# Kernel optimization log

Measured on AMD Instinct MI355X. Metric: run time of the kernel, lower is better.

The kernel has to match this reference:

```python
import jax, jax.numpy as jnp
import numpy as np

# SpargeAttn / spas_sage2_attn_meansim block sizes
BLKQ, BLKK = 128, 64
NUM_HEADS = 8
SIMTHRESHD1 = 0.6
CDFTHRESHD = 0.98


def _block_meta(t, blk):
    # t: [B,H,S,D] -> block means [B,H,nb,D] and min-cosine-to-mean per block [B,H,nb]
    B, H, S, D = t.shape
    nb = S // blk
    tb = t.reshape(B, H, nb, blk, D)
    m = tb.mean(axis=3)
    tn = tb / (jnp.linalg.norm(tb, axis=-1, keepdims=True) + 1e-6)
    mn = m / (jnp.linalg.norm(m, axis=-1, keepdims=True) + 1e-6)
    cos = jnp.einsum('bhnkd,bhnd->bhnk', tn, mn)
    return m, cos.min(axis=-1)


def _meansim_sparse_attention(q, k, v, scale):
    # Block-sparse attention with mean-similarity pruning (SpargeAttn meansim).
    qm, qsim = _block_meta(q, BLKQ)          # [B,H,nq,D], [B,H,nq]
    km, ksim = _block_meta(k, BLKK)          # [B,H,nk,D], [B,H,nk]
    q_self = qsim > SIMTHRESHD1              # self-similar Q blocks -> mean is representative
    k_self = ksim > SIMTHRESHD1
    # pooled attention map over block means
    pooled = jax.nn.softmax(jnp.einsum('bhqd,bhkd->bhqk', qm, km) * scale, axis=-1)
    # per Q-block row: keep highest-prob K blocks until cumulative mass >= cdfthreshd
    order = jnp.argsort(-pooled, axis=-1)
    sp = jnp.take_along_axis(pooled, order, axis=-1)
    csum = jnp.cumsum(sp, axis=-1)
    keep_sorted = (csum - sp) < CDFTHRESHD   # always keeps at least the top block
    inv = jnp.argsort(order, axis=-1)
    keep = jnp.take_along_axis(keep_sorted, inv, axis=-1)  # [B,H,nq,nk]
    # conservative fallback: non-self-similar Q/K blocks are never pruned
    block_mask = keep | (~q_self)[..., None] | (~k_self)[:, :, None, :]
    tok_mask = jnp.repeat(jnp.repeat(block_mask, BLKQ, axis=2), BLKK, axis=3)
    s = jnp.einsum('bhqd,bhkd->bhqk', q, k) * scale
    s = jnp.where(tok_mask, s, -jnp.inf)
    p = jax.nn.softmax(s, axis=-1)
    return jnp.einsum('bhqk,bhkd->bhqd', p, v)


def setup_inputs() -> dict:
    key = jax.random.key(0)
    B, L, C = 2, 2048, 512
    ks = jax.random.split(key, 3)
    x = jax.random.normal(ks[0], (B, L, C), jnp.float32)
    Wqkv = jax.random.normal(ks[1], (C, 3 * C), jnp.float32) * (C ** -0.5)
    bqkv = jnp.zeros((3 * C,), jnp.float32)
    Wproj = jax.random.normal(ks[2], (C, C), jnp.float32) * (C ** -0.5)
    bproj = jnp.zeros((C,), jnp.float32)
    return {"x": x, "Wqkv": Wqkv, "bqkv": bqkv, "Wproj": Wproj, "bproj": bproj}


def reference(x, Wqkv, bqkv, Wproj, bproj):
    B, L, C = x.shape
    H = NUM_HEADS
    D = C // H
    scale = D ** -0.5
    qkv = (x @ Wqkv + bqkv).reshape(B, L, 3, H, D)
    qkv = jnp.transpose(qkv, (2, 0, 3, 1, 4))  # [3,B,H,L,D]
    q, k, v = qkv[0], qkv[1], qkv[2]
    o = _meansim_sparse_attention(q, k, v, scale)  # [B,H,L,D]
    o = jnp.transpose(o, (0, 2, 1, 3)).reshape(B, L, C)
    return o @ Wproj + bproj
```

## Files before the change

### kernel.cpp

```cpp
#include <hip/hip_runtime.h>
#include <math.h>

typedef unsigned short ushortT;
typedef unsigned int uintT;
typedef __attribute__((ext_vector_type(8))) short short8;
typedef __attribute__((ext_vector_type(16))) float f32x16;
#define MFMA32(a, b, c) __builtin_amdgcn_mfma_f32_32x32x16_bf16((a), (b), (c), 0, 0, 0)


#define LOG2E 1.4426950408889634f

static __device__ __forceinline__ ushortT f2b(float f) {
    union { float f; uintT u; } v; v.f = f;
    uintT u = v.u;
    u += 0x7fffu + ((u >> 16) & 1u);
    return (ushortT)(u >> 16);
}
static __device__ __forceinline__ uintT pack2(float a, float b) {
    return (uintT)f2b(a) | ((uintT)f2b(b) << 16);
}
static __device__ __forceinline__ uintT pack2t(float a, float b) {
    union { float f; uintT u; } x0, x1; x0.f = a; x1.f = b;
    return __builtin_amdgcn_perm(x1.u, x0.u, 0x07060302u);
}
static __device__ __forceinline__ float blo(uintT u) {
    union { uintT u; float f; } v; v.u = u << 16; return v.f;
}
static __device__ __forceinline__ float bhi(uintT u) {
    union { uintT u; float f; } v; v.u = u & 0xffff0000u; return v.f;
}
static __device__ __forceinline__ f32x16 zero16() {
    f32x16 z;
    #pragma unroll
    for (int i = 0; i < 16; ++i) z[i] = 0.f;
    return z;
}

#define NQB 16
#define NKB 32

__global__ __launch_bounds__(256) void prep_kernel(
    const float* __restrict__ x, ushortT* __restrict__ xb,
    const float* __restrict__ Wq, ushortT* __restrict__ Wqt,
    const float* __restrict__ Wp, ushortT* __restrict__ Wpt) {
    const int bid = blockIdx.x, t = threadIdx.x;
    __shared__ float tile[32][33];
    if (bid < 2048) {
        int i = (bid * 256 + t) * 4;
        float4 v = *(const float4*)(x + i);
        uint2 o; o.x = pack2(v.x, v.y); o.y = pack2(v.z, v.w);
        *(uint2*)(xb + i) = o;
        return;
    }
    const float* W; ushortT* Wt; int C, c0, r0;
    if (bid < 2816) {
        const int b = bid - 2048;
        W = Wq; Wt = Wqt; C = 1536;
        c0 = (b % 48) * 32; r0 = (b / 48) * 32;
    } else {
        const int b = bid - 2816;
        W = Wp; Wt = Wpt; C = 512;
        c0 = (b & 15) * 32; r0 = (b >> 4) * 32;
    }
    const int tx = t & 31, ty = t >> 5;
    #pragma unroll
    for (int i = 0; i < 4; ++i)
        tile[ty + 8 * i][tx] = W[(size_t)(r0 + ty + 8 * i) * C + c0 + tx];
    __syncthreads();
    #pragma unroll
    for (int i = 0; i < 4; ++i) {
        int rr = ty + 8 * i;
        Wt[(size_t)(c0 + rr) * 512 + r0 + tx] = f2b(tile[tx][rr]);
    }
}

__global__ __launch_bounds__(256) void qkv_gemm_kernel(
    const ushortT* __restrict__ xb, const ushortT* __restrict__ wt,
    const float* __restrict__ bias,
    ushortT* __restrict__ qb, ushortT* __restrict__ kfrag, ushortT* __restrict__ vfrag,
    float* __restrict__ qm, float* __restrict__ km,
    float* __restrict__ qs, float* __restrict__ ks) {
    __shared__ __align__(16) ushortT As[2][128 * 40];
    __shared__ __align__(16) ushortT Bs[2][64 * 40];
    __shared__ float sumbuf[4][64];
    __shared__ float meanS[2][64];
    __shared__ float wminS[4];
    const int t = threadIdx.x;
    const int l = t & 63, w = t >> 6;
    const int lm = l & 31, lh = l >> 5;
    const int rowbase = blockIdx.y * 128;
    const int colbase = blockIdx.x * 64;

    f32x16 acc[2];
    acc[0] = zero16(); acc[1] = zero16();

    const int r = t >> 1, half = t & 1;
    const ushortT* Ag = xb + (size_t)(rowbase + r) * 512 + half * 16;
    const int soA = r * 40 + half * 16;
    const int rb = t >> 2, q4 = t & 3;
    const ushortT* Bg = wt + (size_t)(colbase + rb) * 512 + q4 * 8;
    const int soB = rb * 40 + q4 * 8;

    uint4 a0, a1, b0;
    a0 = *(const uint4*)(Ag); a1 = *(const uint4*)(Ag + 8);
    b0 = *(const uint4*)(Bg);
    *(uint4*)(&As[0][soA]) = a0; *(uint4*)(&As[0][soA] + 8) = a1;
    *(uint4*)(&Bs[0][soB]) = b0;

    for (int k0 = 0; k0 < 512; k0 += 32) {
        const int cur = (k0 >> 5) & 1;
        __syncthreads();
        if (k0 < 480) {
            a0 = *(const uint4*)(Ag + k0 + 32); a1 = *(const uint4*)(Ag + k0 + 40);
            b0 = *(const uint4*)(Bg + k0 + 32);
        }
        #pragma unroll
        for (int ks2 = 0; ks2 < 2; ++ks2) {
            const int ko = 16 * ks2 + 8 * lh;
            short8 af  = *(const short8*)(&As[cur][(32 * w + lm) * 40 + ko]);
            short8 b_0 = *(const short8*)(&Bs[cur][lm * 40 + ko]);
            short8 b_1 = *(const short8*)(&Bs[cur][(32 + lm) * 40 + ko]);
            acc[0] = MFMA32(af, b_0, acc[0]);
            acc[1] = MFMA32(af, b_1, acc[1]);
        }
        if (k0 < 480) {
            const int nxt = cur ^ 1;
            *(uint4*)(&As[nxt][soA]) = a0; *(uint4*)(&As[nxt][soA] + 8) = a1;
            *(uint4*)(&Bs[nxt][soB]) = b0;
        }
    }

    const int which = blockIdx.x >> 3;
    const int h = blockIdx.x & 7;
    const int by = blockIdx.y;
    const int b = by >> 4;
    const size_t hb = (size_t)(b * 8 + h);
    float bias2[2];
    #pragma unroll
    for (int nt = 0; nt < 2; ++nt) bias2[nt] = bias[colbase + 32 * nt + lm];
    float msum[2] = {0.f, 0.f};
    #pragma unroll
    for (int nt = 0; nt < 2; ++nt) {
        const int dd = 32 * nt + lm;
        #pragma unroll
        for (int rg = 0; rg < 16; ++rg) {
            const int row_local = 32 * w + (rg & 3) + 8 * (rg >> 2) + 4 * lh;
            const int ll = (rowbase + row_local) & 2047;
            float val = acc[nt][rg] + bias2[nt];
            if (which == 0) {
                val *= 0.125f;
                msum[nt] += val;
                qb[(hb * 2048 + ll) * 64 + dd] = f2b(val * LOG2E);
            } else if (which == 1) {
                msum[nt] += val;
                const int koff = (((ll >> 6) * 8 + ((ll >> 5) & 1) * 4 + (dd >> 4)) << 9)
                               + (((ll & 31) + 32 * ((dd >> 3) & 1)) << 3) + (dd & 7);
                kfrag[hb * 131072 + koff] = f2b(val);
            } else {
                const int voff = (((ll >> 6) * 8 + (dd >> 5) * 4 + ((ll >> 4) & 3)) << 9)
                               + (((dd & 31) + 32 * ((ll >> 3) & 1)) << 3) + (ll & 7);
                vfrag[hb * 131072 + voff] = f2b(val);
            }
            acc[nt][rg] = val;
        }
    }
    if (which == 2) return;
    #pragma unroll
    for (int nt = 0; nt < 2; ++nt) {
        float s = msum[nt] + __shfl_xor(msum[nt], 32);
        if (l < 32) sumbuf[w][32 * nt + lm] = s;
    }
    __syncthreads();
    if (which == 0) {
        if (t < 64) {
            const int qbi = by & 15;
            const float m =
                (sumbuf[0][t] + sumbuf[1][t] + sumbuf[2][t] + sumbuf[3][t]) * (1.0f / 128.0f);
            qm[(hb * 16 + qbi) * 64 + t] = m;
            meanS[0][t] = m;
        }
    } else {
        if (t < 128) {
            const int d = t & 63, pair = t >> 6;
            const int kbi = 2 * (by & 15) + pair;
            const float m =
                (sumbuf[2 * pair][d] + sumbuf[2 * pair + 1][d]) * (1.0f / 64.0f);
            km[(hb * 32 + kbi) * 64 + d] = m;
            meanS[pair][d] = m;
        }
    }
    __syncthreads();
    {
        const int mrow = (which == 0) ? 0 : (w >> 1);
        const float mv0 = meanS[mrow][lm], mv1 = meanS[mrow][32 + lm];
        float mn2 = mv0 * mv0 + mv1 * mv1;
        #pragma unroll
        for (int off = 1; off < 32; off <<= 1) mn2 += __shfl_xor(mn2, off);
        const float mnorm = sqrtf(mn2);
        float cmin = 1e30f;
        #pragma unroll
        for (int rg = 0; rg < 16; ++rg) {
            float dp = acc[0][rg] * mv0 + acc[1][rg] * mv1;
            float nn = acc[0][rg] * acc[0][rg] + acc[1][rg] * acc[1][rg];
            #pragma unroll
            for (int off = 1; off < 32; off <<= 1) {
                dp += __shfl_xor(dp, off);
                nn += __shfl_xor(nn, off);
            }
            const float cosv = dp / ((sqrtf(nn) + 1e-6f) * (mnorm + 1e-6f));
            cmin = fminf(cmin, cosv);
        }
        cmin = fminf(cmin, __shfl_xor(cmin, 32));
        if (l == 0) wminS[w] = cmin;
    }
    __syncthreads();
    if (t == 0) {
        if (which == 0) {
            qs[hb * 16 + (by & 15)] =
                fminf(fminf(wminS[0], wminS[1]), fminf(wminS[2], wminS[3]));
        } else {
            ks[hb * 32 + 2 * (by & 15)]     = fminf(wminS[0], wminS[1]);
            ks[hb * 32 + 2 * (by & 15) + 1] = fminf(wminS[2], wminS[3]);
        }
    }
}

__global__ __launch_bounds__(512, 2) void attn_kernel(
    const ushortT* __restrict__ qb, const ushortT* __restrict__ kfrag,
    const ushortT* __restrict__ vfrag,
    const float* __restrict__ qm, const float* __restrict__ km,
    const float* __restrict__ qs, const float* __restrict__ ks,
    ushortT* __restrict__ ob) {
    __shared__ __align__(16) uint4 ox[6 * 8 * 64];
    __shared__ float lx[6 * 2 * 32];
    __shared__ int klist[33];
    __shared__ float qmS[64];
    __shared__ float pnS[32];

    const int t = threadIdx.x;
    const int l = t & 63, w = t >> 6;
    const int lm = l & 31, lh = l >> 5;
    const int qc = w >> 2, kq = w & 3;
    const int bh = blockIdx.x, qt = blockIdx.y;

    if (t < 64) qmS[t] = qm[((size_t)bh * 16 + qt) * 64 + t];

    const ushortT* qg = qb + ((size_t)bh * 2048 + qt * 128) * 64;
    short8 qf[4][2];
    #pragma unroll
    for (int qh = 0; qh < 2; ++qh)
        #pragma unroll
        for (int ksd = 0; ksd < 4; ++ksd)
            qf[ksd][qh] = *(const short8*)(qg + (64 * qc + 32 * qh + lm) * 64 + 16 * ksd + 8 * lh);
    __syncthreads();

    if (w == 0 && l < 32) {
        const float* kmr = km + ((size_t)bh * 32 + l) * 64;
        float dot = 0.f;
        #pragma unroll
        for (int d = 0; d < 64; ++d) dot += qmS[d] * kmr[d];
        float mx = dot;
        #pragma unroll
        for (int off = 1; off < 32; off <<= 1) mx = fmaxf(mx, __shfl_xor(mx, off));
        const float e = expf(dot - mx);
        float sum = e;
        #pragma unroll
        for (int off = 1; off < 32; off <<= 1) sum += __shfl_xor(sum, off);
        const float pn = e * (1.0f / sum);
        pnS[l] = pn;
        float before = 0.f;
        #pragma unroll
        for (int j = 0; j < 32; ++j) {
            const float pj = pnS[j];
            if (pj > pn || (pj == pn && j < l)) before += pj;
        }
        const bool qfb = !(qs[bh * 16 + qt] > 0.6f);
        const bool kfb = !(ks[bh * 32 + l] > 0.6f);
        const bool keep = (before < 0.98f) || qfb || kfb;
        unsigned long long bal = __ballot(keep);
        if (keep) {
            const int rank = __popcll(bal & ((1ULL << l) - 1ULL));
            klist[rank] = l;
        }
        if (l == 0) klist[32] = __popcll(bal);
    }
    __syncthreads();

    const int cnt = klist[32];
    const ushortT* kfb = kfrag + (size_t)bh * 131072;
    const ushortT* vfb = vfrag + (size_t)bh * 131072;

    f32x16 oacc[2][2];
    oacc[0][0] = zero16(); oacc[1][0] = zero16();
    oacc[0][1] = zero16(); oacc[1][1] = zero16();
    float l_i[2] = {0.f, 0.f};

    for (int j = kq; j < cnt; j += 4) {
        const int kb = klist[j];
        const ushortT* kbase = kfb + kb * 4096;
        const ushortT* vbase = vfb + kb * 4096;
        #pragma unroll
        for (int kh = 0; kh < 2; ++kh) {
            f32x16 sacc[2];
            sacc[0] = zero16(); sacc[1] = zero16();
            #pragma unroll
            for (int ksd = 0; ksd < 4; ++ksd) {
                short8 kf = *(const short8*)(kbase + ((kh * 4 + ksd) << 9) + l * 8);
                sacc[0] = MFMA32(kf, qf[ksd][0], sacc[0]);
                sacc[1] = MFMA32(kf, qf[ksd][1], sacc[1]);
            }
            uintT uu[2][4][2];
            #pragma unroll
            for (int qh = 0; qh < 2; ++qh) {
                float psum0 = 0.f, psum1 = 0.f;
                #pragma unroll
                for (int rp = 0; rp < 8; ++rp) {
                    const float e0 = __builtin_amdgcn_exp2f(sacc[qh][2 * rp]);
                    const float e1 = __builtin_amdgcn_exp2f(sacc[qh][2 * rp + 1]);
                    psum0 += e0; psum1 += e1;
                    uu[qh][rp >> 1][rp & 1] = pack2t(e0, e1);
                }
                float psum = psum0 + psum1;
                psum += __shfl_xor(psum, 32);
                l_i[qh] += psum;
            }
            #pragma unroll
            for (int ksk = 0; ksk < 2; ++ksk) {
                const int ksl = 2 * kh + ksk;
                short8 vf0 = *(const short8*)(vbase + (ksl << 9) + l * 8);
                short8 vf1 = *(const short8*)(vbase + ((4 + ksl) << 9) + l * 8);
                #pragma unroll
                for (int qh = 0; qh < 2; ++qh) {
                    const uintT kA = lh ? uu[qh][2 * ksk + 1][0] : uu[qh][2 * ksk][0];
                    const uintT kB = lh ? uu[qh][2 * ksk + 1][1] : uu[qh][2 * ksk][1];
                    const uintT sA = lh ? uu[qh][2 * ksk][0] : uu[qh][2 * ksk + 1][0];
                    const uintT sB = lh ? uu[qh][2 * ksk][1] : uu[qh][2 * ksk + 1][1];
                    const uintT rA = (uintT)__shfl_xor((int)sA, 32);
                    const uintT rB = (uintT)__shfl_xor((int)sB, 32);
                    union { uintT u[4]; short8 v; } cv;
                    if (lh == 0) { cv.u[0] = kA; cv.u[1] = kB; cv.u[2] = rA; cv.u[3] = rB; }
                    else         { cv.u[0] = rA; cv.u[1] = rB; cv.u[2] = kA; cv.u[3] = kB; }
                    oacc[0][qh] = MFMA32(vf0, cv.v, oacc[0][qh]);
                    oacc[1][qh] = MFMA32(vf1, cv.v, oacc[1][qh]);
                }
            }
        }
    }

    if (kq != 0) {
        const int wslot = qc * 3 + (kq - 1);
        #pragma unroll
        for (int dt = 0; dt < 2; ++dt)
            #pragma unroll
            for (int qh = 0; qh < 2; ++qh)
                #pragma unroll
                for (int g2 = 0; g2 < 2; ++g2) {
                    uint4 u;
                    u.x = pack2(oacc[dt][qh][8 * g2 + 0], oacc[dt][qh][8 * g2 + 1]);
                    u.y = pack2(oacc[dt][qh][8 * g2 + 2], oacc[dt][qh][8 * g2 + 3]);
                    u.z = pack2(oacc[dt][qh][8 * g2 + 4], oacc[dt][qh][8 * g2 + 5]);
                    u.w = pack2(oacc[dt][qh][8 * g2 + 6], oacc[dt][qh][8 * g2 + 7]);
                    ox[(wslot * 8 + (dt * 4 + qh * 2 + g2)) * 64 + l] = u;
                }
        if (lh == 0) {
            lx[(wslot * 2 + 0) * 32 + lm] = l_i[0];
            lx[(wslot * 2 + 1) * 32 + lm] = l_i[1];
        }
    }
    __syncthreads();
    if (kq == 0) {
        float lt[2] = {l_i[0], l_i[1]};
        #pragma unroll
        for (int p = 0; p < 3; ++p) {
            const int ws2 = qc * 3 + p;
            lt[0] += lx[(ws2 * 2 + 0) * 32 + lm];
            lt[1] += lx[(ws2 * 2 + 1) * 32 + lm];
            #pragma unroll
            for (int dt = 0; dt < 2; ++dt)
                #pragma unroll
                for (int qh = 0; qh < 2; ++qh)
                    #pragma unroll
                    for (int g2 = 0; g2 < 2; ++g2) {
                        uint4 u = ox[(ws2 * 8 + (dt * 4 + qh * 2 + g2)) * 64 + l];
                        oacc[dt][qh][8 * g2 + 0] += blo(u.x);
                        oacc[dt][qh][8 * g2 + 1] += bhi(u.x);
                        oacc[dt][qh][8 * g2 + 2] += blo(u.y);
                        oacc[dt][qh][8 * g2 + 3] += bhi(u.y);
                        oacc[dt][qh][8 * g2 + 4] += blo(u.z);
                        oacc[dt][qh][8 * g2 + 5] += bhi(u.z);
                        oacc[dt][qh][8 * g2 + 6] += blo(u.w);
                        oacc[dt][qh][8 * g2 + 7] += bhi(u.w);
                    }
        }
        #pragma unroll
        for (int qh = 0; qh < 2; ++qh) {
            const float inv = 1.0f / lt[qh];
            const int token = qt * 128 + qc * 64 + 32 * qh + lm;
            ushortT* orow = ob + ((size_t)bh * 2048 + token) * 64;
            #pragma unroll
            for (int dt = 0; dt < 2; ++dt)
                #pragma unroll
                for (int rp = 0; rp < 8; ++rp) {
                    const int d0 = 32 * dt + 8 * (rp >> 1) + 4 * lh + 2 * (rp & 1);
                    *(uintT*)(orow + d0) =
                        pack2(oacc[dt][qh][2 * rp] * inv, oacc[dt][qh][2 * rp + 1] * inv);
                }
        }
    }
}

__global__ __launch_bounds__(256) void proj_gemm_kernel(
    const ushortT* __restrict__ ob, const ushortT* __restrict__ wpt,
    const float* __restrict__ bias, float* __restrict__ out) {
    __shared__ __align__(16) ushortT As[2][64 * 40];
    __shared__ __align__(16) ushortT Bs[2][64 * 40];
    const int t = threadIdx.x;
    const int l = t & 63, w = t >> 6;
    const int lm = l & 31, lh = l >> 5;
    const int rh = w & 1, ch = w >> 1;
    const int rowbase = blockIdx.y * 64;
    const int colbase = blockIdx.x * 64;

    f32x16 acc = zero16();

    const int r = t >> 2, q4 = t & 3;
    const int token = rowbase + r;
    const int b2 = token >> 11, lt = token & 2047;
    const int so = r * 40 + q4 * 8;
    const ushortT* obbase = ob + ((size_t)(b2 * 8) * 2048 + lt) * 64 + q4 * 8;
    const ushortT* Bg = wpt + (size_t)(colbase + r) * 512 + q4 * 8;

    uint4 a0, b0;
    a0 = *(const uint4*)(obbase);
    b0 = *(const uint4*)(Bg);
    *(uint4*)(&As[0][so]) = a0;
    *(uint4*)(&Bs[0][so]) = b0;

    for (int k0 = 0; k0 < 512; k0 += 32) {
        const int cur = (k0 >> 5) & 1;
        __syncthreads();
        if (k0 < 480) {
            const int kn = k0 + 32;
            const ushortT* Ag = obbase + (size_t)(kn >> 6) * 131072 + (kn & 63);
            a0 = *(const uint4*)(Ag);
            b0 = *(const uint4*)(Bg + kn);
        }
        #pragma unroll
        for (int ks2 = 0; ks2 < 2; ++ks2) {
            const int ko = 16 * ks2 + 8 * lh;
            short8 af = *(const short8*)(&As[cur][(32 * rh + lm) * 40 + ko]);
            short8 bf = *(const short8*)(&Bs[cur][(32 * ch + lm) * 40 + ko]);
            acc = MFMA32(af, bf, acc);
        }
        if (k0 < 480) {
            const int nxt = cur ^ 1;
            *(uint4*)(&As[nxt][so]) = a0;
            *(uint4*)(&Bs[nxt][so]) = b0;
        }
    }
    const int c = colbase + 32 * ch + lm;
    const float bb = bias[c];
    #pragma unroll
    for (int rg = 0; rg < 16; ++rg) {
        const int row_local = 32 * rh + (rg & 3) + 8 * (rg >> 2) + 4 * lh;
        out[(size_t)(rowbase + row_local) * 512 + c] = acc[rg] + bb;
    }
}

extern "C" void kernel_launch(void* const* d_in, const int* in_sizes, int n_in,
                              void* d_out, int out_size, void* d_ws, size_t ws_size,
                              hipStream_t stream) {
    const float* x     = (const float*)d_in[0];
    const float* Wqkv  = (const float*)d_in[1];
    const float* bqkv  = (const float*)d_in[2];
    const float* Wproj = (const float*)d_in[3];
    const float* bproj = (const float*)d_in[4];
    float* out = (float*)d_out;

    char* w = (char*)d_ws;
    ushortT* xb     = (ushortT*)(w);
    ushortT* wqkvt  = (ushortT*)(w + 4194304);
    ushortT* wprojt = (ushortT*)(w + 5767168);
    ushortT* qb     = (ushortT*)(w + 6291456);
    ushortT* kfrag  = (ushortT*)(w + 10485760);
    ushortT* vfrag  = (ushortT*)(w + 14680064);
    ushortT* ob     = (ushortT*)(w + 18874368);
    float*   qm     = (float*)(w + 23068672);
    float*   km     = (float*)(w + 23134208);
    float*   qs     = (float*)(w + 36406272);
    float*   ks     = (float*)(w + 36407296);

    prep_kernel<<<3072, 256, 0, stream>>>(x, xb, Wqkv, wqkvt, Wproj, wprojt);
    qkv_gemm_kernel<<<dim3(24, 32), 256, 0, stream>>>(xb, wqkvt, bqkv, qb, kfrag, vfrag,
                                                      qm, km, qs, ks);
    attn_kernel<<<dim3(16, 16), 512, 0, stream>>>(qb, kfrag, vfrag, qm, km, qs, ks, ob);
    proj_gemm_kernel<<<dim3(8, 64), 256, 0, stream>>>(ob, wprojt, bproj, out);
}
```

Before: 127.3 us.

## Pre-swizzle x and Wqkv into MFMA fragment layout, drop LDS staging in QKV GEMM

The prep kernel now writes bf16 x and the transposed Wqkv directly in a 32x16 MFMA-fragment-tiled layout. The QKV GEMM then loads A and B fragments straight from global memory with one 16-byte load per lane per k-step. This removes the shared-memory double buffer and its __syncthreads. The cost is that B tiles are re-read from global or L2 by each wave without LDS sharing, and the prep kernel's weight writes become scattered 2-byte stores.

```diff
diff --git a/kernel.cpp b/kernel.cpp
--- a/kernel.cpp
+++ b/kernel.cpp
@@ -40,26 +40,29 @@
 #define NKB 32
 
 __global__ __launch_bounds__(256) void prep_kernel(
-    const float* __restrict__ x, ushortT* __restrict__ xb,
-    const float* __restrict__ Wq, ushortT* __restrict__ Wqt,
+    const float* __restrict__ x, ushortT* __restrict__ xbf,
+    const float* __restrict__ Wq, ushortT* __restrict__ wbf,
     const float* __restrict__ Wp, ushortT* __restrict__ Wpt) {
     const int bid = blockIdx.x, t = threadIdx.x;
     __shared__ float tile[32][33];
     if (bid < 2048) {
-        int i = (bid * 256 + t) * 4;
+        const int i = (bid * 256 + t) * 4;
+        const int row = i >> 9, k = i & 511;
         float4 v = *(const float4*)(x + i);
         uint2 o; o.x = pack2(v.x, v.y); o.y = pack2(v.z, v.w);
-        *(uint2*)(xb + i) = o;
+        const int off = (((row >> 5) * 32 + (k >> 4)) << 9)
+                      + (((row & 31) + 32 * ((k >> 3) & 1)) << 3) + (k & 7);
+        *(uint2*)(xbf + off) = o;
         return;
     }
-    const float* W; ushortT* Wt; int C, c0, r0;
+    const float* W; int C, c0, r0; bool isQkv;
     if (bid < 2816) {
         const int b = bid - 2048;
-        W = Wq; Wt = Wqt; C = 1536;
+        W = Wq; C = 1536; isQkv = true;
         c0 = (b % 48) * 32; r0 = (b / 48) * 32;
     } else {
         const int b = bid - 2816;
-        W = Wp; Wt = Wpt; C = 512;
+        W = Wp; C = 512; isQkv = false;
         c0 = (b & 15) * 32; r0 = (b >> 4) * 32;
     }
     const int tx = t & 31, ty = t >> 5;
@@ -69,19 +72,25 @@
     __syncthreads();
     #pragma unroll
     for (int i = 0; i < 4; ++i) {
-        int rr = ty + 8 * i;
-        Wt[(size_t)(c0 + rr) * 512 + r0 + tx] = f2b(tile[tx][rr]);
+        const int rr = ty + 8 * i;
+        const ushortT val = f2b(tile[tx][rr]);
+        const int n = c0 + rr, k = r0 + tx;
+        if (isQkv) {
+            const int off = (((n >> 5) * 32 + (k >> 4)) << 9)
+                          + (((n & 31) + 32 * ((k >> 3) & 1)) << 3) + (k & 7);
+            wbf[off] = val;
+        } else {
+            Wpt[(size_t)n * 512 + k] = val;
+        }
     }
 }
 
 __global__ __launch_bounds__(256) void qkv_gemm_kernel(
-    const ushortT* __restrict__ xb, const ushortT* __restrict__ wt,
+    const ushortT* __restrict__ xbf, const ushortT* __restrict__ wbf,
     const float* __restrict__ bias,
     ushortT* __restrict__ qb, ushortT* __restrict__ kfrag, ushortT* __restrict__ vfrag,
     float* __restrict__ qm, float* __restrict__ km,
     float* __restrict__ qs, float* __restrict__ ks) {
-    __shared__ __align__(16) ushortT As[2][128 * 40];
-    __shared__ __align__(16) ushortT Bs[2][64 * 40];
     __shared__ float sumbuf[4][64];
     __shared__ float meanS[2][64];
     __shared__ float wminS[4];
@@ -91,43 +100,21 @@
     const int rowbase = blockIdx.y * 128;
     const int colbase = blockIdx.x * 64;
 
+    const int rtile = blockIdx.y * 4 + w;
+    const ushortT* Ab = xbf + ((size_t)rtile << 14);
+    const ushortT* B0 = wbf + ((size_t)(blockIdx.x * 2) << 14);
+    const ushortT* B1 = B0 + (1 << 14);
+
     f32x16 acc[2];
     acc[0] = zero16(); acc[1] = zero16();
 
-    const int r = t >> 1, half = t & 1;
-    const ushortT* Ag = xb + (size_t)(rowbase + r) * 512 + half * 16;
-    const int soA = r * 40 + half * 16;
-    const int rb = t >> 2, q4 = t & 3;
-    const ushortT* Bg = wt + (size_t)(colbase + rb) * 512 + q4 * 8;
-    const int soB = rb * 40 + q4 * 8;
-
-    uint4 a0, a1, b0;
-    a0 = *(const uint4*)(Ag); a1 = *(const uint4*)(Ag + 8);
-    b0 = *(const uint4*)(Bg);
-    *(uint4*)(&As[0][soA]) = a0; *(uint4*)(&As[0][soA] + 8) = a1;
-    *(uint4*)(&Bs[0][soB]) = b0;
-
-    for (int k0 = 0; k0 < 512; k0 += 32) {
-        const int cur = (k0 >> 5) & 1;
-        __syncthreads();
-        if (k0 < 480) {
-            a0 = *(const uint4*)(Ag + k0 + 32); a1 = *(const uint4*)(Ag + k0 + 40);
-            b0 = *(const uint4*)(Bg + k0 + 32);
-        }
-        #pragma unroll
-        for (int ks2 = 0; ks2 < 2; ++ks2) {
-            const int ko = 16 * ks2 + 8 * lh;
-            short8 af  = *(const short8*)(&As[cur][(32 * w + lm) * 40 + ko]);
-            short8 b_0 = *(const short8*)(&Bs[cur][lm * 40 + ko]);
-            short8 b_1 = *(const short8*)(&Bs[cur][(32 + lm) * 40 + ko]);
-            acc[0] = MFMA32(af, b_0, acc[0]);
-            acc[1] = MFMA32(af, b_1, acc[1]);
-        }
-        if (k0 < 480) {
-            const int nxt = cur ^ 1;
-            *(uint4*)(&As[nxt][soA]) = a0; *(uint4*)(&As[nxt][soA] + 8) = a1;
-            *(uint4*)(&Bs[nxt][soB]) = b0;
-        }
+    #pragma unroll 4
+    for (int ks2 = 0; ks2 < 32; ++ks2) {
+        short8 af = *(const short8*)(Ab + (ks2 << 9) + l * 8);
+        short8 b0 = *(const short8*)(B0 + (ks2 << 9) + l * 8);
+        short8 b1 = *(const short8*)(B1 + (ks2 << 9) + l * 8);
+        acc[0] = MFMA32(af, b0, acc[0]);
+        acc[1] = MFMA32(af, b1, acc[1]);
     }
 
     const int which = blockIdx.x >> 3;
@@ -478,8 +465,8 @@
     float* out = (float*)d_out;
 
     char* w = (char*)d_ws;
-    ushortT* xb     = (ushortT*)(w);
-    ushortT* wqkvt  = (ushortT*)(w + 4194304);
+    ushortT* xbf    = (ushortT*)(w);
+    ushortT* wbf    = (ushortT*)(w + 4194304);
     ushortT* wprojt = (ushortT*)(w + 5767168);
     ushortT* qb     = (ushortT*)(w + 6291456);
     ushortT* kfrag  = (ushortT*)(w + 10485760);
@@ -490,8 +477,8 @@
     float*   qs     = (float*)(w + 36406272);
     float*   ks     = (float*)(w + 36407296);
 
-    prep_kernel<<<3072, 256, 0, stream>>>(x, xb, Wqkv, wqkvt, Wproj, wprojt);
-    qkv_gemm_kernel<<<dim3(24, 32), 256, 0, stream>>>(xb, wqkvt, bqkv, qb, kfrag, vfrag,
+    prep_kernel<<<3072, 256, 0, stream>>>(x, xbf, Wqkv, wbf, Wproj, wprojt);
+    qkv_gemm_kernel<<<dim3(24, 32), 256, 0, stream>>>(xbf, wbf, bqkv, qb, kfrag, vfrag,
                                                       qm, km, qs, ks);
     attn_kernel<<<dim3(16, 16), 512, 0, stream>>>(qb, kfrag, vfrag, qm, km, qs, ks, ob);
     proj_gemm_kernel<<<dim3(8, 64), 256, 0, stream>>>(ob, wprojt, bproj, out);
```

New measurement: 128.8 us. Within noise of the previous version (+1.1%).
